# Kernel tuning notes

Hardware: AMD Instinct MI355X
Metric: run time of the kernel (lower is better)

## Reference

```python
import jax, jax.numpy as jnp
import numpy as np

D_MODEL = 2048
N_HEAD = 32
N_KV_HEAD = 8
HEAD_DIM = D_MODEL // N_HEAD  # 64
N_REP = N_HEAD // N_KV_HEAD   # 4
B, T = 2, 2048


def setup_inputs() -> dict:
    key = jax.random.key(0)
    ks = jax.random.split(key, 5)
    s = 0.02
    return {
        "x": jax.random.normal(ks[0], (B, T, D_MODEL), dtype=jnp.float32),
        "Wq": jax.random.normal(ks[1], (D_MODEL, N_HEAD * HEAD_DIM), dtype=jnp.float32) * s,
        "Wk": jax.random.normal(ks[2], (D_MODEL, N_KV_HEAD * HEAD_DIM), dtype=jnp.float32) * s,
        "Wv": jax.random.normal(ks[3], (D_MODEL, N_KV_HEAD * HEAD_DIM), dtype=jnp.float32) * s,
        "Wo": jax.random.normal(ks[4], (N_HEAD * HEAD_DIM, D_MODEL), dtype=jnp.float32) * s,
        "mask": 1,
    }


def _rope_tables(t_len, dim, dtype):
    inv_freq = 1.0 / (10000.0 ** (jnp.arange(0, dim, 2, dtype=jnp.float32) / dim))
    freqs = jnp.arange(t_len, dtype=jnp.float32)[:, None] * inv_freq[None, :]  # [T, dim/2]
    return jnp.cos(freqs).astype(dtype), jnp.sin(freqs).astype(dtype)


def _apply_rope(x, cos, sin):
    # x: [B, H, T, D]; cos/sin: [T, D/2]; half-concat layout as in source
    x1, x2 = x[..., ::2], x[..., 1::2]
    return jnp.concatenate([x1 * cos - x2 * sin, x1 * sin + x2 * cos], axis=-1)


def reference(x, Wq, Wk, Wv, Wo, mask):
    b, t, c = x.shape
    q = (x @ Wq).reshape(b, t, N_HEAD, HEAD_DIM).transpose(0, 2, 1, 3)      # [B,H,T,D]
    k = (x @ Wk).reshape(b, t, N_KV_HEAD, HEAD_DIM).transpose(0, 2, 1, 3)   # [B,Hkv,T,D]
    v = (x @ Wv).reshape(b, t, N_KV_HEAD, HEAD_DIM).transpose(0, 2, 1, 3)
    cos, sin = _rope_tables(t, HEAD_DIM, x.dtype)
    q = _apply_rope(q, cos, sin)
    k = _apply_rope(k, cos, sin)
    k = jnp.repeat(k, N_REP, axis=1)  # [B,H,T,D]
    v = jnp.repeat(v, N_REP, axis=1)
    scale = 1.0 / np.sqrt(HEAD_DIM)
    scores = jnp.einsum('bhtd,bhsd->bhts', q, k) * scale  # [B,H,T,T]
    if mask:
        causal = jnp.tril(jnp.ones((t, t), dtype=bool))
        scores = jnp.where(causal, scores, jnp.float32(-jnp.inf).astype(scores.dtype))
    weights = jax.nn.softmax(scores, axis=-1)
    out = jnp.einsum('bhts,bhsd->bhtd', weights, v)        # [B,H,T,D]
    out = out.transpose(0, 2, 1, 3).reshape(b, t, c)
    return out @ Wo
```

## Files before the change

kernel.cpp:

```cpp
#include <hip/hip_runtime.h>
#include <stdint.h>

#define D_MODEL 2048
#define N_HEAD 32
#define N_KV_HEAD 8
#define HEAD_DIM 64
#define BATCH 2
#define SEQ 2048
#define ROWS (BATCH*SEQ)
#define QKV_N 3072
#define SCL2F 0.18033688011112042f

typedef __attribute__((ext_vector_type(4))) float f32x4;
typedef __attribute__((ext_vector_type(8))) short bf16x8;

__device__ __forceinline__ float bflo(unsigned u){ return __uint_as_float(u << 16); }
__device__ __forceinline__ float bfhi(unsigned u){ return __uint_as_float(u & 0xFFFF0000u); }
__device__ __forceinline__ unsigned f2bf(float f){
  unsigned u = __float_as_uint(f);
  u += 0x7FFFu + ((u >> 16) & 1u);
  return u >> 16;
}
__device__ __forceinline__ unsigned cvtpk(float a, float b){
  unsigned r;
  asm("v_cvt_pk_bf16_f32 %0, %1, %2" : "=v"(r) : "v"(a), "v"(b));
  return r;
}

__device__ __forceinline__ void async_copy16(const void* g, void* lds){
  __builtin_amdgcn_global_load_lds(
      (const __attribute__((address_space(1))) void*)g,
      (__attribute__((address_space(3))) void*)lds, 16, 0, 0);
}

__global__ __launch_bounds__(256) void k_prep(const float* __restrict__ x,
                                              const float* __restrict__ Wq,
                                              const float* __restrict__ Wk,
                                              const float* __restrict__ Wv,
                                              const float* __restrict__ Wo,
                                              unsigned short* __restrict__ xb,
                                              unsigned short* __restrict__ Wqkvt,
                                              unsigned short* __restrict__ Wot,
                                              float* __restrict__ ct,
                                              float* __restrict__ st){
  __shared__ float tile[64][65];
  const int bid = blockIdx.x;
  const int tid = threadIdx.x;
  if (bid < 8192) {
    int i = bid*256 + tid;
    float4 v = ((const float4*)x)[i];
    unsigned lo = f2bf(v.x) | (f2bf(v.y) << 16);
    unsigned hi = f2bf(v.z) | (f2bf(v.w) << 16);
    ((uint2*)xb)[i] = make_uint2(lo, hi);
    return;
  }
  if (bid < 10752) {
    const int rel0 = bid - 8192;
    const float* W; unsigned short* Wt; int N; int rel;
    if (rel0 < 1024)      { W = Wq; Wt = Wqkvt;                         N = 2048; rel = rel0; }
    else if (rel0 < 1280) { W = Wk; Wt = Wqkvt + (size_t)2048*D_MODEL;  N = 512;  rel = rel0 - 1024; }
    else if (rel0 < 1536) { W = Wv; Wt = Wqkvt + (size_t)2560*D_MODEL;  N = 512;  rel = rel0 - 1280; }
    else                  { W = Wo; Wt = Wot;                           N = 2048; rel = rel0 - 1536; }
    const int ntn = N >> 6;
    const int tk = rel / ntn, tn = rel % ntn;
    #pragma unroll
    for (int i = 0; i < 4; ++i) {
      int idx4 = tid + 256*i;
      int r = idx4 >> 4;
      int c4 = idx4 & 15;
      float4 v = *(const float4*)(W + (size_t)(tk*64 + r)*N + tn*64 + c4*4);
      tile[r][c4*4+0] = v.x; tile[r][c4*4+1] = v.y;
      tile[r][c4*4+2] = v.z; tile[r][c4*4+3] = v.w;
    }
    __syncthreads();
    #pragma unroll
    for (int i = 0; i < 8; ++i) {
      int o2 = tid + 256*i;
      int n  = o2 >> 5;
      int k2 = o2 & 31;
      unsigned lo = f2bf(tile[k2*2+0][n]);
      unsigned hi = f2bf(tile[k2*2+1][n]);
      *(unsigned*)(Wt + (size_t)(tn*64 + n)*D_MODEL + tk*64 + k2*2) = lo | (hi << 16);
    }
    return;
  }
  {
    int gid = (bid - 10752)*256 + tid;
    int t = gid >> 5, d = gid & 31;
    float inv = exp2f(-13.287712379549449f * ((float)d * (1.0f/32.0f)));
    float a = (float)t * inv;
    ct[gid] = cosf(a);
    st[gid] = sinf(a);
  }
}

__global__ __launch_bounds__(256) void k_ropek(unsigned short* __restrict__ QKVb,
                                               const float* __restrict__ ct,
                                               const float* __restrict__ st){
  int gid = blockIdx.x*256 + threadIdx.x;
  int row = gid >> 3;
  int h = gid & 7;
  int t = row & (SEQ-1);
  unsigned* p = (unsigned*)(QKVb + (size_t)row*QKV_N + 2048 + h*HEAD_DIM);
  float o1[32], o2[32];
  #pragma unroll
  for (int d = 0; d < 32; ++d) {
    unsigned u = p[d];
    float x1 = bflo(u), x2 = bfhi(u);
    float c = ct[t*32+d], s = st[t*32+d];
    o1[d] = x1*c - x2*s;
    o2[d] = x1*s + x2*c;
  }
  #pragma unroll
  for (int i = 0; i < 16; ++i) {
    p[i]    = f2bf(o1[2*i]) | (f2bf(o1[2*i+1]) << 16);
    p[16+i] = f2bf(o2[2*i]) | (f2bf(o2[2*i+1]) << 16);
  }
}

template<int MREP, bool VSPLIT, typename OUT_T>
__global__ __launch_bounds__(512, 1) void k_gemm8(const unsigned short* __restrict__ A,
                                                  const unsigned short* __restrict__ Bt,
                                                  OUT_T* __restrict__ C,
                                                  unsigned short* __restrict__ Vt,
                                                  int M, int N, int K){
  constexpr int BM = MREP*32;
  constexpr int ABYTES = BM*128;
  constexpr int AHALF  = BM*64;
  constexpr int BUF = ABYTES + 32768;
  constexpr int LA = MREP/4;
  constexpr int VMW = 6 + 2*LA;

  __shared__ __align__(16) char smem[2*BUF];

  const int nbn = N >> 8;
  const int bswz = ((int)blockIdx.x & 7)*((int)gridDim.x >> 3) + ((int)blockIdx.x >> 3);
  const int m0 = (bswz / nbn) * BM;
  const int n0 = (bswz % nbn) * 256;
  const int tid = threadIdx.x;
  const int wid = tid >> 6, lane = tid & 63;
  const int wm = wid >> 2, wn = wid & 3;
  const int fr = lane & 15, q = lane >> 4;
  const int NT = K >> 6;
  const int NITER = NT >> 1;
  const size_t rb = (size_t)K*2;

  f32x4 acc[MREP][4] = {};
  bf16x8 Bfrag[4];

  const int srow = tid >> 2, sq = tid & 3;

  auto stageA = [&](int t, int ks, int bufb){
    #pragma unroll
    for (int r = 0; r < LA; ++r){
      int row = r*128 + srow;
      int sw = ((row >> 1) & 3);
      async_copy16((const char*)A + (size_t)(m0+row)*rb + t*128 + ks*64 + ((sq ^ sw)*16),
                   smem + bufb + ks*AHALF + (r*512 + tid)*16);
    }
  };
  auto stageB = [&](int t, int ks, int bufb){
    #pragma unroll
    for (int r = 0; r < 2; ++r){
      int row = r*128 + srow;
      int sw = ((row >> 1) & 3);
      async_copy16((const char*)Bt + (size_t)(n0+row)*rb + t*128 + ks*64 + ((sq ^ sw)*16),
                   smem + bufb + ABYTES + ks*16384 + (r*512 + tid)*16);
    }
  };

#define PHASE(KS, MH, BUFB, LOADB, STAGE_STMT, DO_VMCNT) {                              \
    bf16x8 Af[MREP/2];                                                                  \
    _Pragma("unroll")                                                                   \
    for (int mm = 0; mm < MREP/2; ++mm){                                                \
      int row = wm*(MREP*16) + ((MH)*(MREP/2)+mm)*16 + fr;                              \
      Af[mm] = *(const bf16x8*)(smem + (BUFB) + (KS)*AHALF + row*64 +                   \
                                ((q ^ ((row>>1)&3))*16));                               \
    }                                                                                   \
    if (LOADB){                                                                         \
      _Pragma("unroll")                                                                 \
      for (int n = 0; n < 4; ++n){                                                      \
        int row = wn*64 + n*16 + fr;                                                    \
        Bfrag[n] = *(const bf16x8*)(smem + (BUFB) + ABYTES + (KS)*16384 + row*64 +      \
                                    ((q ^ ((row>>1)&3))*16));                           \
      }                                                                                 \
    }                                                                                   \
    STAGE_STMT;                                                                         \
    __builtin_amdgcn_s_barrier();                                                       \
    __builtin_amdgcn_s_setprio(1);                                                      \
    _Pragma("unroll")                                                                   \
    for (int mm = 0; mm < MREP/2; ++mm)                                                 \
      _Pragma("unroll")                                                                 \
      for (int n = 0; n < 4; ++n)                                                       \
        acc[(MH)*(MREP/2)+mm][n] = __builtin_amdgcn_mfma_f32_16x16x32_bf16(             \
            Af[mm], Bfrag[n], acc[(MH)*(MREP/2)+mm][n], 0, 0, 0);                       \
    __builtin_amdgcn_s_setprio(0);                                                      \
    if (DO_VMCNT) asm volatile("s_waitcnt vmcnt(%0)" :: "n"(VMW) : "memory");           \
    __builtin_amdgcn_s_barrier();                                                       \
  }

  stageB(0, 0, 0);  stageA(0, 0, 0);  stageB(0, 1, 0);  stageA(0, 1, 0);
  stageB(1, 0, BUF); stageA(1, 0, BUF); stageB(1, 1, BUF);
  asm volatile("s_waitcnt vmcnt(%0)" :: "n"(VMW) : "memory");
  __builtin_amdgcn_s_barrier();

  for (int i = 0; i < NITER; ++i){
    const int t2 = (2*i+2) & (NT-1);
    const int t3 = (2*i+3) & (NT-1);
    PHASE(0, 0, 0,   true,  stageA(2*i+1, 1, BUF), false)
    PHASE(0, 1, 0,   false, stageB(t2, 0, 0),      true)
    PHASE(1, 0, 0,   true,  stageA(t2, 0, 0),      false)
    PHASE(1, 1, 0,   false, stageB(t2, 1, 0),      true)
    PHASE(0, 0, BUF, true,  stageA(t2, 1, 0),      false)
    PHASE(0, 1, BUF, false, stageB(t3, 0, BUF),    true)
    PHASE(1, 0, BUF, true,  stageA(t3, 0, BUF),    false)
    PHASE(1, 1, BUF, false, stageB(t3, 1, BUF),    true)
  }
#undef PHASE

  asm volatile("s_waitcnt vmcnt(0)" ::: "memory");
  const bool isV = VSPLIT && (n0 >= 2560);
  if (isV) {
    #pragma unroll
    for (int m = 0; m < MREP; ++m){
      int grow = m0 + wm*(MREP*16) + m*16 + q*4;
      int bb = grow >> 11, sv = grow & (SEQ-1);
      #pragma unroll
      for (int n = 0; n < 4; ++n){
        int cn = n0 + wn*64 + n*16 + fr - 2560;
        int kvh = cn >> 6, d = cn & 63;
        uint2 w = { cvtpk(acc[m][n][0], acc[m][n][1]), cvtpk(acc[m][n][2], acc[m][n][3]) };
        *(uint2*)(Vt + ((size_t)((bb*8 + kvh)*64 + d))*SEQ + sv) = w;
      }
    }
    return;
  }
  #pragma unroll
  for (int m = 0; m < MREP; ++m){
    #pragma unroll
    for (int n = 0; n < 4; ++n){
      size_t base = (size_t)(m0 + wm*(MREP*16) + m*16 + q*4)*N + (n0 + wn*64 + n*16 + fr);
      #pragma unroll
      for (int j = 0; j < 4; ++j){
        float v = acc[m][n][j];
        if constexpr (sizeof(OUT_T) == 2)
          ((unsigned short*)C)[base + (size_t)j*N] = (unsigned short)f2bf(v);
        else
          ((float*)C)[base + (size_t)j*N] = v;
      }
    }
  }
}

__global__ __launch_bounds__(256) void k_attn_mfma(const unsigned short* __restrict__ Q,
                                                   const unsigned short* __restrict__ Kb,
                                                   const unsigned short* __restrict__ Vt,
                                                   unsigned short* __restrict__ O,
                                                   const int* __restrict__ maskp,
                                                   const float* __restrict__ ct,
                                                   const float* __restrict__ st){
  __shared__ __align__(16) char smem[32768];
  char* Vsm = smem + 16384;
  const int orig = blockIdx.x;
  const int bid = (orig & 7)*128 + (orig >> 3);
  const int jj = bid & 15;
  const int h  = (bid >> 4) & 31;
  const int b  = bid >> 9;
  const int kvh = h >> 2;
  const int tid = threadIdx.x;
  const int wid = tid >> 6, lane = tid & 63;
  const int q_ = lane & 15, g = lane >> 4;
  char* Psm = smem + 24576 + wid*2048;
  const bool causal = (maskp[0] != 0);

  bf16x8 onesf;
  #pragma unroll
  for (int e = 0; e < 8; ++e) onesf[e] = (short)0x3F80;

  auto stageK = [&](int tile, int bufbase){
    const int s0s = tile*64;
    #pragma unroll
    for (int it = 0; it < 2; ++it) {
      int i = (wid*2+it)*64 + lane;
      int s = i >> 3, c = i & 7;
      async_copy16(Kb + (size_t)(b*SEQ + s0s + s)*QKV_N + kvh*HEAD_DIM + ((c ^ (s&7))*8),
                   smem + bufbase + (wid*2+it)*1024);
    }
  };
  auto stageV = [&](int tile){
    const int s0s = tile*64;
    #pragma unroll
    for (int it = 0; it < 2; ++it) {
      int i = (wid*2+it)*64 + lane;
      int s = i >> 3, c = i & 7;
      async_copy16(Vt + ((size_t)(b*N_KV_HEAD + kvh)*HEAD_DIM + s)*SEQ + s0s + ((c ^ (s&7))*8),
                   Vsm + (wid*2+it)*1024);
    }
  };

  for (int pass = 0; pass < 2; ++pass) {
    const int qt = pass ? jj : (31 - jj);
    const int q0 = qt*64;
    const int qg = q0 + 16*wid + q_;
    const int nt = causal ? (qt+1) : (SEQ/64);

    bf16x8 qf0, qf1;
    {
      const int trow = qg;
      const unsigned short* qsrc = Q + (size_t)(b*SEQ + trow)*QKV_N + h*HEAD_DIM + g*16;
      union { bf16x8 h; unsigned u[4]; } xa, xb;
      xa.h = *(const bf16x8*)(qsrc);
      xb.h = *(const bf16x8*)(qsrc + 8);
      const float4* cp = (const float4*)(ct + trow*32 + g*8);
      const float4* sp = (const float4*)(st + trow*32 + g*8);
      float4 c0 = cp[0], c1 = cp[1];
      float4 s0 = sp[0], s1 = sp[1];
      float cc[8] = {c0.x,c0.y,c0.z,c0.w,c1.x,c1.y,c1.z,c1.w};
      float ss[8] = {s0.x,s0.y,s0.z,s0.w,s1.x,s1.y,s1.z,s1.w};
      float e0[8], e1[8];
      #pragma unroll
      for (int e = 0; e < 8; ++e) {
        unsigned u = (e < 4) ? xa.u[e] : xb.u[e-4];
        float x1 = bflo(u), x2 = bfhi(u);
        float cs = cc[e]*SCL2F, sn = ss[e]*SCL2F;
        e0[e] = x1*cs - x2*sn;
        e1[e] = x1*sn + x2*cs;
      }
      union { unsigned u[4]; bf16x8 h; } p0, p1;
      #pragma unroll
      for (int m = 0; m < 4; ++m) {
        p0.u[m] = cvtpk(e0[2*m], e0[2*m+1]);
        p1.u[m] = cvtpk(e1[2*m], e1[2*m+1]);
      }
      qf0 = p0.h; qf1 = p1.h;
    }

    f32x4 acc[4] = {};
    f32x4 accl = {};
    float mrun = -1e30f;

    stageK(0, 0);
    stageV(0);
    asm volatile("s_waitcnt vmcnt(0)" ::: "memory");
    __syncthreads();

    for (int t = 0; t < nt; ++t) {
      const int s0 = t*64;
      const int cur = t & 1;
      const char* Kbuf = smem + cur*8192;

      if (t+1 < nt) stageK(t+1, (cur^1)*8192);

      f32x4 sa[4];
      __builtin_amdgcn_s_setprio(1);
      #pragma unroll
      for (int f = 0; f < 4; ++f) {
        const char* kb = Kbuf + (16*f + q_)*128;
        bf16x8 a0 = *(const bf16x8*)(kb + ((g ^ (q_&7))*16));
        bf16x8 a1 = *(const bf16x8*)(kb + (((g+4) ^ (q_&7))*16));
        f32x4 z = {};
        z = __builtin_amdgcn_mfma_f32_16x16x32_bf16(a0, qf0, z, 0, 0, 0);
        z = __builtin_amdgcn_mfma_f32_16x16x32_bf16(a1, qf1, z, 0, 0, 0);
        sa[f] = z;
      }
      __builtin_amdgcn_s_setprio(0);

      const bool domask = causal && (t == qt);
      float x[4][4];
      float cm[4];
      #pragma unroll
      for (int f = 0; f < 4; ++f) {
        #pragma unroll
        for (int r = 0; r < 4; ++r) {
          float v = sa[f][r];
          if (domask && (s0 + 16*f + 4*g + r > qg)) v = -3.0e38f;
          x[f][r] = v;
        }
        cm[f] = fmaxf(fmaxf(x[f][0], x[f][1]), fmaxf(x[f][2], x[f][3]));
      }
      float cmax = fmaxf(fmaxf(cm[0], cm[1]), fmaxf(cm[2], cm[3]));
      cmax = fmaxf(cmax, __shfl_xor(cmax, 16));
      cmax = fmaxf(cmax, __shfl_xor(cmax, 32));
      if (!__all(cmax <= mrun + 8.0f)) {
        float mnew = fmaxf(mrun, cmax);
        float r2 = exp2f(mrun - mnew);
        #pragma unroll
        for (int m = 0; m < 4; ++m) {
          acc[m][0] *= r2; acc[m][1] *= r2; acc[m][2] *= r2; acc[m][3] *= r2;
        }
        accl[0] *= r2; accl[1] *= r2; accl[2] *= r2; accl[3] *= r2;
        mrun = mnew;
      }
      #pragma unroll
      for (int f = 0; f < 4; ++f) {
        float e0 = exp2f(x[f][0] - mrun);
        float e1 = exp2f(x[f][1] - mrun);
        float e2 = exp2f(x[f][2] - mrun);
        float e3 = exp2f(x[f][3] - mrun);
        uint2 w = { cvtpk(e0, e1), cvtpk(e2, e3) };
        int byteo = q_*128 + (((2*f + (g>>1)) ^ (q_&7))*16) + (g&1)*8;
        *(uint2*)(Psm + byteo) = w;
      }

      asm volatile("s_waitcnt vmcnt(0)" ::: "memory");
      __syncthreads();

      __builtin_amdgcn_s_setprio(1);
      #pragma unroll
      for (int kh = 0; kh < 2; ++kh) {
        bf16x8 pb = *(const bf16x8*)(Psm + q_*128 + (((g + 4*kh) ^ (q_&7))*16));
        accl = __builtin_amdgcn_mfma_f32_16x16x32_bf16(onesf, pb, accl, 0, 0, 0);
        #pragma unroll
        for (int m = 0; m < 4; ++m) {
          bf16x8 va = *(const bf16x8*)(Vsm + (16*m + q_)*128 + (((g + 4*kh) ^ (q_&7))*16));
          acc[m] = __builtin_amdgcn_mfma_f32_16x16x32_bf16(va, pb, acc[m], 0, 0, 0);
        }
      }
      __builtin_amdgcn_s_setprio(0);

      __syncthreads();
      if (t+1 < nt) stageV(t+1);
    }

    float inv = 1.0f / accl[0];
    #pragma unroll
    for (int m = 0; m < 4; ++m) {
      uint2 w = { cvtpk(acc[m][0]*inv, acc[m][1]*inv), cvtpk(acc[m][2]*inv, acc[m][3]*inv) };
      int byteo = q_*128 + (((2*m + (g>>1)) ^ (q_&7))*16) + (g&1)*8;
      *(uint2*)(Psm + byteo) = w;
    }
    #pragma unroll
    for (int cc = 0; cc < 2; ++cc) {
      int row = lane >> 2;
      int ch = (lane & 3)*2 + cc;
      uint4 v = *(const uint4*)(Psm + row*128 + ((ch ^ (row&7))*16));
      *(uint4*)(O + (size_t)(b*SEQ + q0 + 16*wid + row)*D_MODEL + h*HEAD_DIM + ch*8) = v;
    }
  }
}

extern "C" void kernel_launch(void* const* d_in, const int* in_sizes, int n_in,
                              void* d_out, int out_size, void* d_ws, size_t ws_size,
                              hipStream_t stream){
  const float* x  = (const float*)d_in[0];
  const float* Wq = (const float*)d_in[1];
  const float* Wk = (const float*)d_in[2];
  const float* Wv = (const float*)d_in[3];
  const float* Wo = (const float*)d_in[4];
  const int* maskp = (const int*)d_in[5];
  float* out = (float*)d_out;

  char* ws = (char*)d_ws;
  unsigned short* xb    = (unsigned short*)(ws);
  unsigned short* AO    = (unsigned short*)(ws);
  unsigned short* Wqkvt = (unsigned short*)(ws + 16777216);
  unsigned short* Vt    = (unsigned short*)(ws + 16777216);
  unsigned short* Wot   = (unsigned short*)(ws + 29360128);
  unsigned short* QKVb  = (unsigned short*)(ws + 37748736);
  float* ct = (float*)(ws + 62914560);
  float* st = (float*)(ws + 63176704);
  Vt = (unsigned short*)(ws + 63438848);

  k_prep<<<11008, 256, 0, stream>>>(x, Wq, Wk, Wv, Wo, xb, Wqkvt, Wot, ct, st);

  k_gemm8<8, true, unsigned short><<<192, 512, 0, stream>>>(xb, Wqkvt, QKVb, Vt, 4096, QKV_N, 2048);

  k_ropek<<<128, 256, 0, stream>>>(QKVb, ct, st);

  k_attn_mfma<<<BATCH*N_HEAD*16, 256, 0, stream>>>(QKVb, QKVb + 2048, Vt, AO, maskp, ct, st);

  k_gemm8<4, false, float><<<256, 512, 0, stream>>>(AO, Wot, out, (unsigned short*)nullptr, 4096, 2048, 2048);
}
```

Measured before the change: 207.1 us.

## Process paired long and short query tiles in one shared KV loop

The attention kernel used to handle two causal query tiles (31-jj and jj) in two sequential passes, streaming K/V separately for each. Both tiles now share a single KV loop. Each staged K/V tile feeds both query tiles until the short tile's causal limit, which removes the redundant K/V reloads and the extra syncs of the second pass. In exchange the kernel uses more registers and LDS (two accumulator sets and two P buffers), which may reduce occupancy.

```diff
diff --git a/kernel.cpp b/kernel.cpp
--- a/kernel.cpp
+++ b/kernel.cpp
@@ -259,7 +259,7 @@
                                                    const int* __restrict__ maskp,
                                                    const float* __restrict__ ct,
                                                    const float* __restrict__ st){
-  __shared__ __align__(16) char smem[32768];
+  __shared__ __align__(16) char smem[40960];
   char* Vsm = smem + 16384;
   const int orig = blockIdx.x;
   const int bid = (orig & 7)*128 + (orig >> 3);
@@ -270,8 +270,15 @@
   const int tid = threadIdx.x;
   const int wid = tid >> 6, lane = tid & 63;
   const int q_ = lane & 15, g = lane >> 4;
-  char* Psm = smem + 24576 + wid*2048;
+  char* PsmL = smem + 24576 + wid*4096;
+  char* PsmS = PsmL + 2048;
   const bool causal = (maskp[0] != 0);
+
+  const int qtL = 31 - jj, qtS = jj;
+  const int q0L = qtL*64, q0S = qtS*64;
+  const int qgL = q0L + 16*wid + q_;
+  const int qgS = q0S + 16*wid + q_;
+  const int ntL = causal ? (qtL+1) : (SEQ/64);
 
   bf16x8 onesf;
   #pragma unroll
@@ -298,143 +305,208 @@
     }
   };
 
-  for (int pass = 0; pass < 2; ++pass) {
-    const int qt = pass ? jj : (31 - jj);
-    const int q0 = qt*64;
-    const int qg = q0 + 16*wid + q_;
-    const int nt = causal ? (qt+1) : (SEQ/64);
-
-    bf16x8 qf0, qf1;
+  auto ropeq = [&](int qg, bf16x8& f0, bf16x8& f1){
+    const unsigned short* qsrc = Q + (size_t)(b*SEQ + qg)*QKV_N + h*HEAD_DIM + g*16;
+    union { bf16x8 h; unsigned u[4]; } xa, xb;
+    xa.h = *(const bf16x8*)(qsrc);
+    xb.h = *(const bf16x8*)(qsrc + 8);
+    const float4* cp = (const float4*)(ct + qg%SEQ*32 + g*8);
+    const float4* sp = (const float4*)(st + qg%SEQ*32 + g*8);
+    float4 c0 = cp[0], c1 = cp[1];
+    float4 s0 = sp[0], s1 = sp[1];
+    float cc[8] = {c0.x,c0.y,c0.z,c0.w,c1.x,c1.y,c1.z,c1.w};
+    float ss[8] = {s0.x,s0.y,s0.z,s0.w,s1.x,s1.y,s1.z,s1.w};
+    float e0[8], e1[8];
+    #pragma unroll
+    for (int e = 0; e < 8; ++e) {
+      unsigned u = (e < 4) ? xa.u[e] : xb.u[e-4];
+      float x1 = bflo(u), x2 = bfhi(u);
+      float cs = cc[e]*SCL2F, sn = ss[e]*SCL2F;
+      e0[e] = x1*cs - x2*sn;
+      e1[e] = x1*sn + x2*cs;
+    }
+    union { unsigned u[4]; bf16x8 h; } p0, p1;
+    #pragma unroll
+    for (int m = 0; m < 4; ++m) {
+      p0.u[m] = cvtpk(e0[2*m], e0[2*m+1]);
+      p1.u[m] = cvtpk(e1[2*m], e1[2*m+1]);
+    }
+    f0 = p0.h; f1 = p1.h;
+  };
+  bf16x8 qfL0, qfL1, qfS0, qfS1;
+  ropeq(qgL, qfL0, qfL1);
+  ropeq(qgS, qfS0, qfS1);
+
+  f32x4 accL[4] = {}, accS[4] = {};
+  f32x4 acclL = {}, acclS = {};
+  float mL = -1e30f, mS = -1e30f;
+
+  stageK(0, 0);
+  stageV(0);
+  asm volatile("s_waitcnt vmcnt(0)" ::: "memory");
+  __syncthreads();
+
+  for (int t = 0; t < ntL; ++t) {
+    const int s0 = t*64;
+    const int cur = t & 1;
+    const char* Kbuf = smem + cur*8192;
+    const bool bothA = (!causal) || (t <= qtS);
+
+    if (t+1 < ntL) stageK(t+1, (cur^1)*8192);
+
+    f32x4 saL[4], saS[4];
+    __builtin_amdgcn_s_setprio(1);
+    #pragma unroll
+    for (int f = 0; f < 4; ++f) {
+      const char* kb = Kbuf + (16*f + q_)*128;
+      bf16x8 a0 = *(const bf16x8*)(kb + ((g ^ (q_&7))*16));
+      bf16x8 a1 = *(const bf16x8*)(kb + (((g+4) ^ (q_&7))*16));
+      f32x4 zL = {};
+      zL = __builtin_amdgcn_mfma_f32_16x16x32_bf16(a0, qfL0, zL, 0, 0, 0);
+      zL = __builtin_amdgcn_mfma_f32_16x16x32_bf16(a1, qfL1, zL, 0, 0, 0);
+      saL[f] = zL;
+      if (bothA) {
+        f32x4 zS = {};
+        zS = __builtin_amdgcn_mfma_f32_16x16x32_bf16(a0, qfS0, zS, 0, 0, 0);
+        zS = __builtin_amdgcn_mfma_f32_16x16x32_bf16(a1, qfS1, zS, 0, 0, 0);
+        saS[f] = zS;
+      }
+    }
+    __builtin_amdgcn_s_setprio(0);
+
     {
-      const int trow = qg;
-      const unsigned short* qsrc = Q + (size_t)(b*SEQ + trow)*QKV_N + h*HEAD_DIM + g*16;
-      union { bf16x8 h; unsigned u[4]; } xa, xb;
-      xa.h = *(const bf16x8*)(qsrc);
-      xb.h = *(const bf16x8*)(qsrc + 8);
-      const float4* cp = (const float4*)(ct + trow*32 + g*8);
-      const float4* sp = (const float4*)(st + trow*32 + g*8);
-      float4 c0 = cp[0], c1 = cp[1];
-      float4 s0 = sp[0], s1 = sp[1];
-      float cc[8] = {c0.x,c0.y,c0.z,c0.w,c1.x,c1.y,c1.z,c1.w};
-      float ss[8] = {s0.x,s0.y,s0.z,s0.w,s1.x,s1.y,s1.z,s1.w};
-      float e0[8], e1[8];
-      #pragma unroll
-      for (int e = 0; e < 8; ++e) {
-        unsigned u = (e < 4) ? xa.u[e] : xb.u[e-4];
-        float x1 = bflo(u), x2 = bfhi(u);
-        float cs = cc[e]*SCL2F, sn = ss[e]*SCL2F;
-        e0[e] = x1*cs - x2*sn;
-        e1[e] = x1*sn + x2*cs;
-      }
-      union { unsigned u[4]; bf16x8 h; } p0, p1;
-      #pragma unroll
-      for (int m = 0; m < 4; ++m) {
-        p0.u[m] = cvtpk(e0[2*m], e0[2*m+1]);
-        p1.u[m] = cvtpk(e1[2*m], e1[2*m+1]);
-      }
-      qf0 = p0.h; qf1 = p1.h;
-    }
-
-    f32x4 acc[4] = {};
-    f32x4 accl = {};
-    float mrun = -1e30f;
-
-    stageK(0, 0);
-    stageV(0);
-    asm volatile("s_waitcnt vmcnt(0)" ::: "memory");
-    __syncthreads();
-
-    for (int t = 0; t < nt; ++t) {
-      const int s0 = t*64;
-      const int cur = t & 1;
-      const char* Kbuf = smem + cur*8192;
-
-      if (t+1 < nt) stageK(t+1, (cur^1)*8192);
-
-      f32x4 sa[4];
-      __builtin_amdgcn_s_setprio(1);
-      #pragma unroll
-      for (int f = 0; f < 4; ++f) {
-        const char* kb = Kbuf + (16*f + q_)*128;
-        bf16x8 a0 = *(const bf16x8*)(kb + ((g ^ (q_&7))*16));
-        bf16x8 a1 = *(const bf16x8*)(kb + (((g+4) ^ (q_&7))*16));
-        f32x4 z = {};
-        z = __builtin_amdgcn_mfma_f32_16x16x32_bf16(a0, qf0, z, 0, 0, 0);
-        z = __builtin_amdgcn_mfma_f32_16x16x32_bf16(a1, qf1, z, 0, 0, 0);
-        sa[f] = z;
-      }
-      __builtin_amdgcn_s_setprio(0);
-
-      const bool domask = causal && (t == qt);
-      float x[4][4];
+      const bool domask = causal && (t == qtL);
       float cm[4];
       #pragma unroll
       for (int f = 0; f < 4; ++f) {
         #pragma unroll
         for (int r = 0; r < 4; ++r) {
-          float v = sa[f][r];
-          if (domask && (s0 + 16*f + 4*g + r > qg)) v = -3.0e38f;
-          x[f][r] = v;
+          float v = saL[f][r];
+          if (domask && (s0 + 16*f + 4*g + r > qgL)) v = -3.0e38f;
+          saL[f][r] = v;
         }
-        cm[f] = fmaxf(fmaxf(x[f][0], x[f][1]), fmaxf(x[f][2], x[f][3]));
+        cm[f] = fmaxf(fmaxf(saL[f][0], saL[f][1]), fmaxf(saL[f][2], saL[f][3]));
       }
       float cmax = fmaxf(fmaxf(cm[0], cm[1]), fmaxf(cm[2], cm[3]));
       cmax = fmaxf(cmax, __shfl_xor(cmax, 16));
       cmax = fmaxf(cmax, __shfl_xor(cmax, 32));
-      if (!__all(cmax <= mrun + 8.0f)) {
-        float mnew = fmaxf(mrun, cmax);
-        float r2 = exp2f(mrun - mnew);
+      if (!__all(cmax <= mL + 8.0f)) {
+        float mnew = fmaxf(mL, cmax);
+        float r2 = exp2f(mL - mnew);
         #pragma unroll
         for (int m = 0; m < 4; ++m) {
-          acc[m][0] *= r2; acc[m][1] *= r2; acc[m][2] *= r2; acc[m][3] *= r2;
+          accL[m][0] *= r2; accL[m][1] *= r2; accL[m][2] *= r2; accL[m][3] *= r2;
         }
-        accl[0] *= r2; accl[1] *= r2; accl[2] *= r2; accl[3] *= r2;
-        mrun = mnew;
+        acclL[0] *= r2; acclL[1] *= r2; acclL[2] *= r2; acclL[3] *= r2;
+        mL = mnew;
       }
       #pragma unroll
       for (int f = 0; f < 4; ++f) {
-        float e0 = exp2f(x[f][0] - mrun);
-        float e1 = exp2f(x[f][1] - mrun);
-        float e2 = exp2f(x[f][2] - mrun);
-        float e3 = exp2f(x[f][3] - mrun);
+        float e0 = exp2f(saL[f][0] - mL);
+        float e1 = exp2f(saL[f][1] - mL);
+        float e2 = exp2f(saL[f][2] - mL);
+        float e3 = exp2f(saL[f][3] - mL);
         uint2 w = { cvtpk(e0, e1), cvtpk(e2, e3) };
         int byteo = q_*128 + (((2*f + (g>>1)) ^ (q_&7))*16) + (g&1)*8;
-        *(uint2*)(Psm + byteo) = w;
-      }
-
-      asm volatile("s_waitcnt vmcnt(0)" ::: "memory");
-      __syncthreads();
-
-      __builtin_amdgcn_s_setprio(1);
-      #pragma unroll
-      for (int kh = 0; kh < 2; ++kh) {
-        bf16x8 pb = *(const bf16x8*)(Psm + q_*128 + (((g + 4*kh) ^ (q_&7))*16));
-        accl = __builtin_amdgcn_mfma_f32_16x16x32_bf16(onesf, pb, accl, 0, 0, 0);
+        *(uint2*)(PsmL + byteo) = w;
+      }
+    }
+    if (bothA) {
+      const bool domask = causal && (t == qtS);
+      float cm[4];
+      #pragma unroll
+      for (int f = 0; f < 4; ++f) {
+        #pragma unroll
+        for (int r = 0; r < 4; ++r) {
+          float v = saS[f][r];
+          if (domask && (s0 + 16*f + 4*g + r > qgS)) v = -3.0e38f;
+          saS[f][r] = v;
+        }
+        cm[f] = fmaxf(fmaxf(saS[f][0], saS[f][1]), fmaxf(saS[f][2], saS[f][3]));
+      }
+      float cmax = fmaxf(fmaxf(cm[0], cm[1]), fmaxf(cm[2], cm[3]));
+      cmax = fmaxf(cmax, __shfl_xor(cmax, 16));
+      cmax = fmaxf(cmax, __shfl_xor(cmax, 32));
+      if (!__all(cmax <= mS + 8.0f)) {
+        float mnew = fmaxf(mS, cmax);
+        float r2 = exp2f(mS - mnew);
         #pragma unroll
         for (int m = 0; m < 4; ++m) {
-          bf16x8 va = *(const bf16x8*)(Vsm + (16*m + q_)*128 + (((g + 4*kh) ^ (q_&7))*16));
-          acc[m] = __builtin_amdgcn_mfma_f32_16x16x32_bf16(va, pb, acc[m], 0, 0, 0);
+          accS[m][0] *= r2; accS[m][1] *= r2; accS[m][2] *= r2; accS[m][3] *= r2;
         }
-      }
-      __builtin_amdgcn_s_setprio(0);
-
-      __syncthreads();
-      if (t+1 < nt) stageV(t+1);
-    }
-
-    float inv = 1.0f / accl[0];
+        acclS[0] *= r2; acclS[1] *= r2; acclS[2] *= r2; acclS[3] *= r2;
+        mS = mnew;
+      }
+      #pragma unroll
+      for (int f = 0; f < 4; ++f) {
+        float e0 = exp2f(saS[f][0] - mS);
+        float e1 = exp2f(saS[f][1] - mS);
+        float e2 = exp2f(saS[f][2] - mS);
+        float e3 = exp2f(saS[f][3] - mS);
+        uint2 w = { cvtpk(e0, e1), cvtpk(e2, e3) };
+        int byteo = q_*128 + (((2*f + (g>>1)) ^ (q_&7))*16) + (g&1)*8;
+        *(uint2*)(PsmS + byteo) = w;
+      }
+    }
+
+    asm volatile("s_waitcnt vmcnt(0)" ::: "memory");
+    __syncthreads();
+
+    __builtin_amdgcn_s_setprio(1);
+    #pragma unroll
+    for (int kh = 0; kh < 2; ++kh) {
+      int po = q_*128 + (((g + 4*kh) ^ (q_&7))*16);
+      bf16x8 pbL = *(const bf16x8*)(PsmL + po);
+      acclL = __builtin_amdgcn_mfma_f32_16x16x32_bf16(onesf, pbL, acclL, 0, 0, 0);
+      bf16x8 pbS;
+      if (bothA) {
+        pbS = *(const bf16x8*)(PsmS + po);
+        acclS = __builtin_amdgcn_mfma_f32_16x16x32_bf16(onesf, pbS, acclS, 0, 0, 0);
+      }
+      #pragma unroll
+      for (int m = 0; m < 4; ++m) {
+        bf16x8 va = *(const bf16x8*)(Vsm + (16*m + q_)*128 + (((g + 4*kh) ^ (q_&7))*16));
+        accL[m] = __builtin_amdgcn_mfma_f32_16x16x32_bf16(va, pbL, accL[m], 0, 0, 0);
+        if (bothA)
+          accS[m] = __builtin_amdgcn_mfma_f32_16x16x32_bf16(va, pbS, accS[m], 0, 0, 0);
+      }
+    }
+    __builtin_amdgcn_s_setprio(0);
+
+    __syncthreads();
+    if (t+1 < ntL) stageV(t+1);
+  }
+
+  {
+    float inv = 1.0f / acclL[0];
     #pragma unroll
     for (int m = 0; m < 4; ++m) {
-      uint2 w = { cvtpk(acc[m][0]*inv, acc[m][1]*inv), cvtpk(acc[m][2]*inv, acc[m][3]*inv) };
+      uint2 w = { cvtpk(accL[m][0]*inv, accL[m][1]*inv), cvtpk(accL[m][2]*inv, accL[m][3]*inv) };
       int byteo = q_*128 + (((2*m + (g>>1)) ^ (q_&7))*16) + (g&1)*8;
-      *(uint2*)(Psm + byteo) = w;
+      *(uint2*)(PsmL + byteo) = w;
     }
     #pragma unroll
     for (int cc = 0; cc < 2; ++cc) {
       int row = lane >> 2;
       int ch = (lane & 3)*2 + cc;
-      uint4 v = *(const uint4*)(Psm + row*128 + ((ch ^ (row&7))*16));
-      *(uint4*)(O + (size_t)(b*SEQ + q0 + 16*wid + row)*D_MODEL + h*HEAD_DIM + ch*8) = v;
+      uint4 v = *(const uint4*)(PsmL + row*128 + ((ch ^ (row&7))*16));
+      *(uint4*)(O + (size_t)(b*SEQ + q0L + 16*wid + row)*D_MODEL + h*HEAD_DIM + ch*8) = v;
+    }
+  }
+  {
+    float inv = 1.0f / acclS[0];
+    #pragma unroll
+    for (int m = 0; m < 4; ++m) {
+      uint2 w = { cvtpk(accS[m][0]*inv, accS[m][1]*inv), cvtpk(accS[m][2]*inv, accS[m][3]*inv) };
+      int byteo = q_*128 + (((2*m + (g>>1)) ^ (q_&7))*16) + (g&1)*8;
+      *(uint2*)(PsmS + byteo) = w;
+    }
+    #pragma unroll
+    for (int cc = 0; cc < 2; ++cc) {
+      int row = lane >> 2;
+      int ch = (lane & 3)*2 + cc;
+      uint4 v = *(const uint4*)(PsmS + row*128 + ((ch ^ (row&7))*16));
+      *(uint4*)(O + (size_t)(b*SEQ + q0S + 16*wid + row)*D_MODEL + h*HEAD_DIM + ch*8) = v;
     }
   }
 }
@@ -454,12 +526,11 @@
   unsigned short* xb    = (unsigned short*)(ws);
   unsigned short* AO    = (unsigned short*)(ws);
   unsigned short* Wqkvt = (unsigned short*)(ws + 16777216);
-  unsigned short* Vt    = (unsigned short*)(ws + 16777216);
   unsigned short* Wot   = (unsigned short*)(ws + 29360128);
   unsigned short* QKVb  = (unsigned short*)(ws + 37748736);
   float* ct = (float*)(ws + 62914560);
   float* st = (float*)(ws + 63176704);
-  Vt = (unsigned short*)(ws + 63438848);
+  unsigned short* Vt = (unsigned short*)(ws + 63438848);
 
   k_prep<<<11008, 256, 0, stream>>>(x, Wq, Wk, Wv, Wo, xb, Wqkvt, Wot, ct, st);
 
```

Measured after the change: 243.6 us. +17.7%, slower.
